# Kernel tuning notes

Hardware: AMD Instinct MI355X
Metric: run time of the kernel (lower is better)

## Reference

```python
import jax, jax.numpy as jnp
import numpy as np

HEADS = 16
DIM_HEAD = 64
SOFTCAP = 50.0
ROPE_THETA = 10000.0


def setup_inputs() -> dict:
    key = jax.random.key(0)
    ks = jax.random.split(key, 5)
    b, n, d, m, lmax = 2, 2048, 1024, 4, 256
    x = jax.random.normal(ks[0], (b, n, d), dtype=jnp.float32)
    tokens = jax.random.normal(ks[1], (b, m, lmax, d), dtype=jnp.float32)
    offsets = jnp.array([100, 600, 1100, 1600], dtype=jnp.int64)
    modalities = jnp.stack(
        [jnp.zeros_like(offsets), offsets, jnp.full_like(offsets, lmax)], axis=-1
    )  # [m, 3] = (type, offset, length)
    modalities = jnp.broadcast_to(modalities, (b, m, 3))
    gamma = jax.random.normal(ks[2], (d,), dtype=jnp.float32) * 0.02
    w_qkv = jax.random.normal(ks[3], (d, 3 * HEADS * DIM_HEAD), dtype=jnp.float32) / np.sqrt(d)
    w_out = jax.random.normal(ks[4], (HEADS * DIM_HEAD, d), dtype=jnp.float32) / np.sqrt(d)
    return {"x": x, "tokens": tokens, "gamma": gamma, "w_qkv": w_qkv,
            "w_out": w_out, "modalities": modalities}


def _apply_rotary(t, pos):
    # t: [b h n dh], pos: [b n] integer rotary positions (interleaved-pair rotation)
    freqs = 1.0 / (ROPE_THETA ** (jnp.arange(0, DIM_HEAD, 2, dtype=jnp.float32) / DIM_HEAD))
    ang = pos[:, None, :, None].astype(jnp.float32) * freqs  # [b 1 n dh/2]
    cos, sin = jnp.cos(ang), jnp.sin(ang)
    t1, t2 = t[..., ::2], t[..., 1::2]
    out = jnp.stack([t1 * cos - t2 * sin, t1 * sin + t2 * cos], axis=-1)
    return out.reshape(t.shape)


def reference(x, tokens, gamma, w_qkv, w_out, modalities):
    b, n, d = x.shape
    lmax = tokens.shape[2]
    off = modalities[..., 1]   # [b m]
    ln = modalities[..., 2]    # [b m]
    seq = jnp.arange(n)

    # --- embed_modality_tokens: scatter modality tokens into sequence ---
    in_span = (seq[None, None, :] >= off[..., None]) & (seq[None, None, :] < (off + ln)[..., None])  # [b m n]
    is_any = in_span.any(axis=1)  # [b n]
    rel = jnp.clip(seq[None, None, :] - off[..., None], 0, lmax - 1)  # [b m n]
    gathered = jnp.take_along_axis(tokens, rel[..., None], axis=2)  # [b m n d]
    mod_embed = jnp.einsum('bmn,bmnd->bnd', in_span.astype(x.dtype), gathered)
    x = jnp.where(is_any[..., None], mod_embed, x)

    # --- derive_rotary_positions_from_modality_positions (offset=[+1,-1]) ---
    rot_span = (seq[None, None, :] >= (off + 1)[..., None]) & (seq[None, None, :] < (off + ln)[..., None])
    pos = seq[None, :] - jnp.cumsum(rot_span.any(axis=1).astype(jnp.int32), axis=-1)  # [b n]

    # --- naive_attn_mask: causal OR within-modality bidirectional ---
    causal = seq[:, None] >= seq[None, :]  # [i j]
    mod_mask = ((seq[None, None, :, None] >= off[..., None, None]) &
                (seq[None, None, None, :] < (off + ln)[..., None, None])).any(axis=1)  # [b i j]
    mask = causal[None] | mod_mask  # [b i j]

    # --- Attention ---
    scale = DIM_HEAD ** -0.5
    xn = x / jnp.clip(jnp.linalg.norm(x, axis=-1, keepdims=True), 1e-12)
    xn = xn * (d ** 0.5) * (gamma + 1.0)  # RMSNorm (l2norm * sqrt(dim) * (gamma+1))
    qkv = (xn @ w_qkv).reshape(b, n, 3, HEADS, DIM_HEAD)
    q, k, v = (jnp.transpose(qkv[:, :, i], (0, 2, 1, 3)) for i in range(3))  # [b h n dh]
    q = _apply_rotary(q, pos)
    k = _apply_rotary(k, pos)
    scores = jnp.einsum('bhid,bhjd->bhij', q, k) * scale
    scores = jnp.tanh(scores / SOFTCAP) * SOFTCAP  # softclamp
    scores = jnp.where(mask[:, None], scores, -jnp.inf)
    attn = jax.nn.softmax(scores, axis=-1)
    out = jnp.einsum('bhij,bhjd->bhid', attn, v)
    out = jnp.transpose(out, (0, 2, 1, 3)).reshape(b, n, HEADS * DIM_HEAD)
    return out @ w_out
```

## Files before the change

kernel.cpp:

```cpp
#include <hip/hip_runtime.h>
#include <stdint.h>

#define HH 16
#define DHD 64
#define BB 2
#define NN 2048
#define DD 1024
#define MMOD 4
#define LMAX 256
#define BNROWS (BB*NN)
#define QKVN (3*HH*DHD)

typedef __attribute__((ext_vector_type(4))) float f32x4;
typedef __attribute__((ext_vector_type(8))) short s16x8;

__device__ __forceinline__ float bf2f(unsigned short b) {
  return __uint_as_float(((unsigned int)b) << 16);
}
__device__ __forceinline__ unsigned short f2bf(float f) {
  unsigned int u = __float_as_uint(f);
  u += 0x7fffu + ((u >> 16) & 1u);
  return (unsigned short)(u >> 16);
}

#define ASYNC_LDS16(g, l) \
  __builtin_amdgcn_global_load_lds((const __attribute__((address_space(1))) void*)(g), \
                                   (__attribute__((address_space(3))) void*)(l), 16, 0, 0)

__global__ __launch_bounds__(256) void k_prep(const float* __restrict__ x,
                                              const float* __restrict__ tokens,
                                              const float* __restrict__ gamma,
                                              const int* __restrict__ mods,
                                              unsigned short* __restrict__ xn) {
  int bs = blockIdx.x;
  int bb = bs / NN, s = bs % NN;
  int t = threadIdx.x;
  int c = t * 4;
  const float4 xv = *(const float4*)(x + (size_t)bs * DD + c);
  float4 acc = {0.f, 0.f, 0.f, 0.f};
  bool any = false;
  #pragma unroll
  for (int m = 0; m < MMOD; ++m) {
    int off = mods[(bb * MMOD + m) * 3 + 1];
    int ln  = mods[(bb * MMOD + m) * 3 + 2];
    if (s >= off && s < off + ln) {
      any = true;
      int rel = s - off;
      if (rel > LMAX - 1) rel = LMAX - 1;
      if (rel < 0) rel = 0;
      const float4 tv = *(const float4*)(tokens + ((size_t)(bb * MMOD + m) * LMAX + rel) * DD + c);
      acc.x += tv.x; acc.y += tv.y; acc.z += tv.z; acc.w += tv.w;
    }
  }
  float4 v = any ? acc : xv;
  float ss = v.x*v.x + v.y*v.y + v.z*v.z + v.w*v.w;
  #pragma unroll
  for (int o = 32; o; o >>= 1) ss += __shfl_xor(ss, o);
  __shared__ float red[4];
  int wv = t >> 6;
  if ((t & 63) == 0) red[wv] = ss;
  __syncthreads();
  float tot = red[0] + red[1] + red[2] + red[3];
  float norm = sqrtf(tot);
  norm = fmaxf(norm, 1e-12f);
  float sc = 32.0f / norm;
  const float4 g = *(const float4*)(gamma + c);
  unsigned long long pk =
      (unsigned long long)f2bf(v.x * sc * (g.x + 1.f)) |
      ((unsigned long long)f2bf(v.y * sc * (g.y + 1.f)) << 16) |
      ((unsigned long long)f2bf(v.z * sc * (g.z + 1.f)) << 32) |
      ((unsigned long long)f2bf(v.w * sc * (g.w + 1.f)) << 48);
  *(unsigned long long*)(xn + (size_t)bs * DD + c) = pk;
}

__global__ void k_pos(const int* __restrict__ mods, int* __restrict__ pos) {
  int bb = blockIdx.x;
  int lane = threadIdx.x;
  int offs[MMOD], ends[MMOD];
  #pragma unroll
  for (int m = 0; m < MMOD; ++m) {
    int off = mods[(bb * MMOD + m) * 3 + 1];
    int ln  = mods[(bb * MMOD + m) * 3 + 2];
    offs[m] = off + 1;
    ends[m] = off + ln;
  }
  int base = lane * (NN / 64);
  int lc[NN / 64];
  int tot = 0;
  #pragma unroll
  for (int i = 0; i < NN / 64; ++i) {
    int s = base + i;
    int f = 0;
    #pragma unroll
    for (int m = 0; m < MMOD; ++m)
      if (s >= offs[m] && s < ends[m]) f = 1;
    tot += f;
    lc[i] = tot;
  }
  int v = tot;
  #pragma unroll
  for (int o = 1; o < 64; o <<= 1) {
    int u = __shfl_up(v, o);
    if (lane >= o) v += u;
  }
  int excl = v - tot;
  #pragma unroll
  for (int i = 0; i < NN / 64; ++i)
    pos[bb * NN + base + i] = base + i - (excl + lc[i]);
}

__global__ void k_tab(const int* __restrict__ pos, float2* __restrict__ tab) {
  int gid = blockIdx.x * 256 + threadIdx.x;
  int p = gid & 31;
  int bs = gid >> 5;
  float inv = expf(-((float)p / 32.f) * 9.210340371976184f);
  float ang = (float)pos[bs] * inv;
  float sn, cs;
  sincosf(ang, &sn, &cs);
  tab[gid] = make_float2(cs, sn);
}

__global__ void k_tr(const float* __restrict__ in, unsigned short* __restrict__ out,
                     int R, int C) {
  __shared__ float tile[32][33];
  int bx = blockIdx.x, by = blockIdx.y;
  int tx = threadIdx.x, ty = threadIdx.y;
  #pragma unroll
  for (int k = 0; k < 4; ++k) {
    int r = by * 32 + ty + k * 8, c = bx * 32 + tx;
    tile[ty + k * 8][tx] = in[(size_t)r * C + c];
  }
  __syncthreads();
  #pragma unroll
  for (int k = 0; k < 4; ++k) {
    int oc = bx * 32 + ty + k * 8;
    int orr = by * 32 + tx;
    out[(size_t)oc * R + orr] = f2bf(tile[tx][ty + k * 8]);
  }
}

template<bool F32OUT>
__global__ __launch_bounds__(256) void k_gemm(const unsigned short* __restrict__ A,
                                              const unsigned short* __restrict__ Bt,
                                              void* __restrict__ Cp,
                                              int M, int Nn, int K) {
  __shared__ unsigned short As[2][128 * 64];
  __shared__ unsigned short Bs[2][128 * 64];
  int tid = threadIdx.x;
  int lane = tid & 63, wv = tid >> 6;
  int lo = lane & 15, hi = lane >> 4;
  int nb = gridDim.x * gridDim.y;
  int fid = blockIdx.y * gridDim.x + blockIdx.x;
  int cpx = nb >> 3;
  int nid = (fid & 7) * cpx + (fid >> 3);
  int m0 = (nid / gridDim.x) * 128;
  int n0 = (nid % gridDim.x) * 128;
  int wr = wv >> 1, wc = wv & 1;
  f32x4 acc[4][4] = {};

  int srow = tid >> 3;
  int scs  = ((tid & 7) ^ ((tid >> 3) & 7)) * 8;
  #define STAGE_G(BUF, KT) do { \
    _Pragma("unroll") \
    for (int is_ = 0; is_ < 4; ++is_) { \
      int r_ = is_ * 32 + srow; \
      const unsigned short* ga_ = A  + (size_t)(m0 + r_) * K + (KT) + scs; \
      const unsigned short* gb_ = Bt + (size_t)(n0 + r_) * K + (KT) + scs; \
      ASYNC_LDS16(ga_, &As[BUF][(is_ * 256 + wv * 64) * 8]); \
      ASYNC_LDS16(gb_, &Bs[BUF][(is_ * 256 + wv * 64) * 8]); \
    } \
  } while (0)

  int nt = K >> 6;
  STAGE_G(0, 0);
  __syncthreads();
  int buf = 0;
  for (int t = 0; t < nt; ++t) {
    if (t + 1 < nt) STAGE_G(buf ^ 1, (t + 1) << 6);
    #pragma unroll
    for (int ks = 0; ks < 2; ++ks) {
      s16x8 af[4], bfr[4];
      #pragma unroll
      for (int m = 0; m < 4; ++m) {
        int row = wr * 64 + m * 16 + lo;
        int cc = ((ks * 4 + hi) ^ (lo & 7)) * 8;
        af[m] = *(const s16x8*)&As[buf][row * 64 + cc];
      }
      #pragma unroll
      for (int nn = 0; nn < 4; ++nn) {
        int row = wc * 64 + nn * 16 + lo;
        int cc = ((ks * 4 + hi) ^ (lo & 7)) * 8;
        bfr[nn] = *(const s16x8*)&Bs[buf][row * 64 + cc];
      }
      #pragma unroll
      for (int m = 0; m < 4; ++m)
        #pragma unroll
        for (int nn = 0; nn < 4; ++nn)
          acc[m][nn] = __builtin_amdgcn_mfma_f32_16x16x32_bf16(af[m], bfr[nn], acc[m][nn], 0, 0, 0);
    }
    __syncthreads();
    buf ^= 1;
  }

  #pragma unroll
  for (int m = 0; m < 4; ++m) {
    #pragma unroll
    for (int nn = 0; nn < 4; ++nn) {
      int r0 = m0 + wr * 64 + m * 16 + hi * 4;
      int cc = n0 + wc * 64 + nn * 16 + lo;
      #pragma unroll
      for (int j = 0; j < 4; ++j) {
        float val = acc[m][nn][j];
        if (F32OUT) ((float*)Cp)[(size_t)(r0 + j) * Nn + cc] = val;
        else        ((unsigned short*)Cp)[(size_t)(r0 + j) * Nn + cc] = f2bf(val);
      }
    }
  }
}

__global__ __launch_bounds__(256) void k_rope(const unsigned short* __restrict__ qkv,
                                              const float2* __restrict__ tab,
                                              unsigned short* __restrict__ q,
                                              unsigned short* __restrict__ k) {
  int bs = blockIdx.x;
  int bb = bs / NN, s = bs % NN;
  int lane = threadIdx.x & 63, wv = threadIdx.x >> 6;
  #pragma unroll
  for (int g = wv; g < 32; g += 4) {
    int i3 = g >> 4, h = g & 15;
    float val = bf2f(qkv[(size_t)bs * QKVN + g * 64 + lane]);
    float partner = __shfl_xor(val, 1);
    float2 cs = tab[(size_t)bs * 32 + (lane >> 1)];
    float out;
    if ((lane & 1) == 0) out = val * cs.x - partner * cs.y;
    else                 out = partner * cs.y + val * cs.x;
    if (i3 == 0) out *= 0.125f;
    unsigned short* dst = (i3 == 0) ? q : k;
    dst[((size_t)(bb * HH + h) * NN + s) * 64 + lane] = f2bf(out);
  }
}

__global__ __launch_bounds__(256) void k_vtr(const unsigned short* __restrict__ qkvt,
                                             unsigned short* __restrict__ vT) {
  __shared__ unsigned short t[64][72];
  int s0 = blockIdx.x * 64, bh = blockIdx.y, bb = bh >> 4, h = bh & 15;
  int tid = threadIdx.x;
  int r = tid >> 2, c0 = (tid & 3) * 16;
  int cw = c0 ^ (((r >> 4) & 3) << 4);
  const unsigned short* src = qkvt + (size_t)(bb * NN + s0 + r) * QKVN + 2048 + h * 64 + c0;
  *(s16x8*)&t[r][cw]     = *(const s16x8*)src;
  *(s16x8*)&t[r][cw + 8] = *(const s16x8*)(src + 8);
  __syncthreads();
  int dh = tid >> 2, sc = (tid & 3) * 16;
  int col2 = dh ^ ((tid & 3) << 4);
  s16x8 o1, o2;
  #pragma unroll
  for (int i = 0; i < 8; ++i) {
    o1[i] = (short)t[sc + i][col2];
    o2[i] = (short)t[sc + 8 + i][col2];
  }
  unsigned short* dst = vT + ((size_t)bh * 64 + dh) * NN + s0 + sc;
  *(s16x8*)dst       = o1;
  *(s16x8*)(dst + 8) = o2;
}

__global__ __launch_bounds__(512) void k_attn(const unsigned short* __restrict__ q,
                                              const unsigned short* __restrict__ k,
                                              const unsigned short* __restrict__ vT,
                                              const int* __restrict__ mods,
                                              unsigned short* __restrict__ o) {
  __shared__ unsigned short Ks[2][64 * 64];
  __shared__ unsigned short Vs[2][64 * 64];
  __shared__ unsigned short Pw[8][16][72];
  int tid = threadIdx.x;
  int lane = tid & 63, wv = tid >> 6;
  int lo = lane & 15, hi = lane >> 4;

  int fid = blockIdx.y * gridDim.x + blockIdx.x;
  int nid = (fid & 7) * 64 + (fid >> 3);
  int bh = nid >> 4;
  int bx = nid & 15;
  int bb = bh >> 4;
  int q0A = (31 - bx) * 64;
  int q0B = bx * 64;
  int q0w = ((wv < 4) ? q0A : q0B) + (wv & 3) * 16;

  const unsigned short* qb = q + (size_t)bh * NN * 64;
  const unsigned short* kb = k + (size_t)bh * NN * 64;
  const unsigned short* vb = vT + (size_t)bh * 64 * NN;

  s16x8 qf[2];
  {
    int qrow = q0w + lo;
    #pragma unroll
    for (int ks = 0; ks < 2; ++ks)
      qf[ks] = *(const s16x8*)&qb[(size_t)qrow * 64 + ks * 32 + hi * 8];
  }

  int off_[MMOD], end_[MMOD];
  #pragma unroll
  for (int m = 0; m < MMOD; ++m) {
    off_[m] = mods[(bb * MMOD + m) * 3 + 1];
    end_[m] = off_[m] + mods[(bb * MMOD + m) * 3 + 2];
  }
  int limit[4];
  #pragma unroll
  for (int j = 0; j < 4; ++j) {
    int r = q0w + hi * 4 + j;
    int L = r + 1;
    #pragma unroll
    for (int m = 0; m < MMOD; ++m)
      if (off_[m] <= r && end_[m] > L) L = end_[m];
    limit[j] = L;
  }
  int minlim, kvmax_w;
  {
    int L = q0w + 1;
    #pragma unroll
    for (int m = 0; m < MMOD; ++m)
      if (off_[m] <= q0w && end_[m] > L) L = end_[m];
    minlim = L;
    int r = q0w + 15;
    int L2 = r + 1;
    #pragma unroll
    for (int m = 0; m < MMOD; ++m)
      if (off_[m] <= r && end_[m] > L2) L2 = end_[m];
    kvmax_w = L2;
  }
  int nt;
  {
    int ra = q0A + 63;
    int LA = ra + 1;
    #pragma unroll
    for (int m = 0; m < MMOD; ++m)
      if (off_[m] <= ra && end_[m] > LA) LA = end_[m];
    int rb2 = q0B + 63;
    int LB = rb2 + 1;
    #pragma unroll
    for (int m = 0; m < MMOD; ++m)
      if (off_[m] <= rb2 && end_[m] > LB) LB = end_[m];
    int Lblk = (LA > LB) ? LA : LB;
    nt = (Lblk + 63) >> 6;
  }

  #define STAGE_KV(B, KV0) do { \
    int r_ = tid >> 3; \
    int cs_ = (lane & 7) ^ ((lane >> 3) & 7); \
    const unsigned short* gK_ = kb + (size_t)((KV0) + r_) * 64 + cs_ * 8; \
    ASYNC_LDS16(gK_, &Ks[B][wv * 512]); \
    const unsigned short* gV_ = vb + (size_t)r_ * NN + (KV0) + cs_ * 8; \
    ASYNC_LDS16(gV_, &Vs[B][wv * 512]); \
  } while (0)

  float lrunp[4] = {0.f, 0.f, 0.f, 0.f};
  f32x4 accO[4] = {};

  STAGE_KV(0, 0);
  __syncthreads();
  int buf = 0;
  for (int t = 0; t < nt; ++t) {
    if (t + 1 < nt) STAGE_KV(buf ^ 1, (t + 1) << 6);
    int kv0 = t << 6;
    if (kv0 < kvmax_w) {
      f32x4 sv[4];
      #pragma unroll
      for (int cb = 0; cb < 4; ++cb) {
        int krow = cb * 16 + lo;
        int c0 = (hi) ^ (krow & 7);
        int c1 = (4 + hi) ^ (krow & 7);
        s16x8 kf0 = *(const s16x8*)&Ks[buf][krow * 64 + c0 * 8];
        s16x8 kf1 = *(const s16x8*)&Ks[buf][krow * 64 + c1 * 8];
        f32x4 z = {};
        z = __builtin_amdgcn_mfma_f32_16x16x32_bf16(qf[0], kf0, z, 0, 0, 0);
        z = __builtin_amdgcn_mfma_f32_16x16x32_bf16(qf[1], kf1, z, 0, 0, 0);
        sv[cb] = z;
      }

      if (kv0 + 64 <= minlim) {
        #pragma unroll
        for (int cb = 0; cb < 4; ++cb)
          #pragma unroll
          for (int j = 0; j < 4; ++j) {
            float s = sv[cb][j];
            float t2 = s * s;
            float u = __builtin_fmaf(t2, -1.3333333e-4f, 1.0f);
            float cap = __builtin_amdgcn_fmed3f(s * u, -50.f, 50.f);
            float p = __expf(cap);
            lrunp[j] += p;
            Pw[wv][hi * 4 + j][cb * 16 + lo] =
                (unsigned short)(__float_as_uint(p) >> 16);
          }
      } else {
        #pragma unroll
        for (int cb = 0; cb < 4; ++cb) {
          int col = kv0 + cb * 16 + lo;
          #pragma unroll
          for (int j = 0; j < 4; ++j) {
            float s = sv[cb][j];
            float t2 = s * s;
            float u = __builtin_fmaf(t2, -1.3333333e-4f, 1.0f);
            float cap = __builtin_amdgcn_fmed3f(s * u, -50.f, 50.f);
            float p = __expf(cap);
            if (col >= limit[j]) p = 0.f;
            lrunp[j] += p;
            Pw[wv][hi * 4 + j][cb * 16 + lo] =
                (unsigned short)(__float_as_uint(p) >> 16);
          }
        }
      }

      #pragma unroll
      for (int ks = 0; ks < 2; ++ks) {
        s16x8 pa = *(const s16x8*)&Pw[wv][lo][ks * 32 + hi * 8];
        #pragma unroll
        for (int cb = 0; cb < 4; ++cb) {
          int vrow = cb * 16 + lo;
          int vc = (ks * 4 + hi) ^ (vrow & 7);
          s16x8 vf = *(const s16x8*)&Vs[buf][vrow * 64 + vc * 8];
          accO[cb] = __builtin_amdgcn_mfma_f32_16x16x32_bf16(pa, vf, accO[cb], 0, 0, 0);
        }
      }
    }
    __syncthreads();
    buf ^= 1;
  }

  #pragma unroll
  for (int o2 = 1; o2 < 16; o2 <<= 1)
    #pragma unroll
    for (int j = 0; j < 4; ++j) lrunp[j] += __shfl_xor(lrunp[j], o2);

  int h = bh & 15;
  float rl[4];
  #pragma unroll
  for (int j = 0; j < 4; ++j) rl[j] = __builtin_amdgcn_rcpf(lrunp[j]);
  #pragma unroll
  for (int cb = 0; cb < 4; ++cb)
    #pragma unroll
    for (int j = 0; j < 4; ++j) {
      int r = q0w + hi * 4 + j;
      float val = accO[cb][j] * rl[j];
      o[((size_t)(bb * NN) + r) * (HH * DHD) + h * 64 + cb * 16 + lo] = f2bf(val);
    }
}

extern "C" void kernel_launch(void* const* d_in, const int* in_sizes, int n_in,
                              void* d_out, int out_size, void* d_ws, size_t ws_size,
                              hipStream_t stream) {
  (void)in_sizes; (void)n_in; (void)out_size; (void)ws_size;
  const float* x      = (const float*)d_in[0];
  const float* tokens = (const float*)d_in[1];
  const float* gamma  = (const float*)d_in[2];
  const float* w_qkv  = (const float*)d_in[3];
  const float* w_out  = (const float*)d_in[4];
  const int*   mods   = (const int*)d_in[5];

  char* ws = (char*)d_ws;
  unsigned short* xn    = (unsigned short*)(ws + 0);
  unsigned short* wqkvT = (unsigned short*)(ws + 8388608);
  unsigned short* woutT = (unsigned short*)(ws + 14680064);
  unsigned short* qkvt  = (unsigned short*)(ws + 16777216);
  unsigned short* qd    = (unsigned short*)(ws + 41943040);
  unsigned short* kd    = (unsigned short*)(ws + 50331648);
  unsigned short* vTd   = (unsigned short*)(ws + 58720256);
  unsigned short* attno = (unsigned short*)(ws + 67108864);
  int*            pos   = (int*)(ws + 75497472);
  float2*         tab   = (float2*)(ws + 75513856);

  k_prep<<<BNROWS, 256, 0, stream>>>(x, tokens, gamma, mods, xn);
  k_pos<<<BB, 64, 0, stream>>>(mods, pos);
  k_tab<<<(BB * NN * 32) / 256, 256, 0, stream>>>(pos, tab);
  k_tr<<<dim3(QKVN / 32, DD / 32), dim3(32, 8), 0, stream>>>(w_qkv, wqkvT, DD, QKVN);
  k_tr<<<dim3((HH * DHD) / 32, DD / 32), dim3(32, 8), 0, stream>>>(w_out, woutT, HH * DHD, DD);
  k_gemm<false><<<dim3(QKVN / 128, BNROWS / 128), 256, 0, stream>>>(xn, wqkvT, (void*)qkvt, BNROWS, QKVN, DD);
  k_rope<<<BNROWS, 256, 0, stream>>>(qkvt, tab, qd, kd);
  k_vtr<<<dim3(NN / 64, BB * HH), 256, 0, stream>>>(qkvt, vTd);
  k_attn<<<dim3(16, BB * HH), 512, 0, stream>>>(qd, kd, vTd, mods, attno);
  k_gemm<true><<<dim3(DD / 128, BNROWS / 128), 256, 0, stream>>>(attno, woutT, d_out, BNROWS, DD, DD);
}
```

Before: 138.3 us.

## Keep attention probabilities in registers via transposed QK MFMA, dropping LDS P staging

```diff
diff --git a/kernel.cpp b/kernel.cpp
--- a/kernel.cpp
+++ b/kernel.cpp
@@ -13,6 +13,7 @@
 
 typedef __attribute__((ext_vector_type(4))) float f32x4;
 typedef __attribute__((ext_vector_type(8))) short s16x8;
+typedef __attribute__((ext_vector_type(4))) short s16x4;
 
 __device__ __forceinline__ float bf2f(unsigned short b) {
   return __uint_as_float(((unsigned int)b) << 16);
@@ -21,6 +22,11 @@
   unsigned int u = __float_as_uint(f);
   u += 0x7fffu + ((u >> 16) & 1u);
   return (unsigned short)(u >> 16);
+}
+__device__ __forceinline__ unsigned int cvt_pk_bf16(float a, float b) {
+  unsigned int r;
+  asm("v_cvt_pk_bf16_f32 %0, %1, %2" : "=v"(r) : "v"(a), "v"(b));
+  return r;
 }
 
 #define ASYNC_LDS16(g, l) \
@@ -234,7 +240,7 @@
     float out;
     if ((lane & 1) == 0) out = val * cs.x - partner * cs.y;
     else                 out = partner * cs.y + val * cs.x;
-    if (i3 == 0) out *= 0.125f;
+    if (i3 == 0) out *= 0.18033688011112042f;
     unsigned short* dst = (i3 == 0) ? q : k;
     dst[((size_t)(bb * HH + h) * NN + s) * 64 + lane] = f2bf(out);
   }
@@ -271,7 +277,6 @@
                                               unsigned short* __restrict__ o) {
   __shared__ unsigned short Ks[2][64 * 64];
   __shared__ unsigned short Vs[2][64 * 64];
-  __shared__ unsigned short Pw[8][16][72];
   int tid = threadIdx.x;
   int lane = tid & 63, wv = tid >> 6;
   int lo = lane & 15, hi = lane >> 4;
@@ -303,15 +308,14 @@
     off_[m] = mods[(bb * MMOD + m) * 3 + 1];
     end_[m] = off_[m] + mods[(bb * MMOD + m) * 3 + 2];
   }
-  int limit[4];
-  #pragma unroll
-  for (int j = 0; j < 4; ++j) {
-    int r = q0w + hi * 4 + j;
+  int limit_l;
+  {
+    int r = q0w + lo;
     int L = r + 1;
     #pragma unroll
     for (int m = 0; m < MMOD; ++m)
       if (off_[m] <= r && end_[m] > L) L = end_[m];
-    limit[j] = L;
+    limit_l = L;
   }
   int minlim, kvmax_w;
   {
@@ -352,7 +356,7 @@
     ASYNC_LDS16(gV_, &Vs[B][wv * 512]); \
   } while (0)
 
-  float lrunp[4] = {0.f, 0.f, 0.f, 0.f};
+  float lr = 0.f;
   f32x4 accO[4] = {};
 
   STAGE_KV(0, 0);
@@ -363,6 +367,7 @@
     int kv0 = t << 6;
     if (kv0 < kvmax_w) {
       f32x4 sv[4];
+      __builtin_amdgcn_s_setprio(1);
       #pragma unroll
       for (int cb = 0; cb < 4; ++cb) {
         int krow = cb * 16 + lo;
@@ -371,69 +376,67 @@
         s16x8 kf0 = *(const s16x8*)&Ks[buf][krow * 64 + c0 * 8];
         s16x8 kf1 = *(const s16x8*)&Ks[buf][krow * 64 + c1 * 8];
         f32x4 z = {};
-        z = __builtin_amdgcn_mfma_f32_16x16x32_bf16(qf[0], kf0, z, 0, 0, 0);
-        z = __builtin_amdgcn_mfma_f32_16x16x32_bf16(qf[1], kf1, z, 0, 0, 0);
+        z = __builtin_amdgcn_mfma_f32_16x16x32_bf16(kf0, qf[0], z, 0, 0, 0);
+        z = __builtin_amdgcn_mfma_f32_16x16x32_bf16(kf1, qf[1], z, 0, 0, 0);
         sv[cb] = z;
       }
-
-      if (kv0 + 64 <= minlim) {
+      __builtin_amdgcn_s_setprio(0);
+
+      unsigned int pk_[4][2];
+      bool edge = (kv0 + 64 > minlim);
+      int kb0 = kv0 + hi * 4;
+      #pragma unroll
+      for (int cb = 0; cb < 4; ++cb) {
+        float p[4];
         #pragma unroll
-        for (int cb = 0; cb < 4; ++cb)
-          #pragma unroll
-          for (int j = 0; j < 4; ++j) {
-            float s = sv[cb][j];
-            float t2 = s * s;
-            float u = __builtin_fmaf(t2, -1.3333333e-4f, 1.0f);
-            float cap = __builtin_amdgcn_fmed3f(s * u, -50.f, 50.f);
-            float p = __expf(cap);
-            lrunp[j] += p;
-            Pw[wv][hi * 4 + j][cb * 16 + lo] =
-                (unsigned short)(__float_as_uint(p) >> 16);
-          }
-      } else {
+        for (int j = 0; j < 4; ++j) {
+          float s = sv[cb][j];
+          float u = __builtin_fmaf(s * s, -6.40604e-5f, 1.0f);
+          float pp = __builtin_amdgcn_exp2f(s * u);
+          if (edge && (kb0 + cb * 16 + j) >= limit_l) pp = 0.f;
+          p[j] = pp;
+        }
+        lr += (p[0] + p[1]) + (p[2] + p[3]);
+        pk_[cb][0] = cvt_pk_bf16(p[0], p[1]);
+        pk_[cb][1] = cvt_pk_bf16(p[2], p[3]);
+      }
+
+      union { unsigned int u[4]; s16x8 v; } pa0, pa1;
+      pa0.u[0] = pk_[0][0]; pa0.u[1] = pk_[0][1];
+      pa0.u[2] = pk_[1][0]; pa0.u[3] = pk_[1][1];
+      pa1.u[0] = pk_[2][0]; pa1.u[1] = pk_[2][1];
+      pa1.u[2] = pk_[3][0]; pa1.u[3] = pk_[3][1];
+
+      __builtin_amdgcn_s_setprio(1);
+      #pragma unroll
+      for (int ks = 0; ks < 2; ++ks) {
+        s16x8 pa = ks ? pa1.v : pa0.v;
+        int c16 = 4 * ks + (hi >> 1);
+        int sub = (hi & 1) * 4;
         #pragma unroll
-        for (int cb = 0; cb < 4; ++cb) {
-          int col = kv0 + cb * 16 + lo;
-          #pragma unroll
-          for (int j = 0; j < 4; ++j) {
-            float s = sv[cb][j];
-            float t2 = s * s;
-            float u = __builtin_fmaf(t2, -1.3333333e-4f, 1.0f);
-            float cap = __builtin_amdgcn_fmed3f(s * u, -50.f, 50.f);
-            float p = __expf(cap);
-            if (col >= limit[j]) p = 0.f;
-            lrunp[j] += p;
-            Pw[wv][hi * 4 + j][cb * 16 + lo] =
-                (unsigned short)(__float_as_uint(p) >> 16);
-          }
+        for (int cbo = 0; cbo < 4; ++cbo) {
+          int dh = cbo * 16 + lo;
+          int base = dh * 64 + sub;
+          s16x4 vA = *(const s16x4*)&Vs[buf][base + ((c16 ^ (dh & 7)) << 3)];
+          s16x4 vB = *(const s16x4*)&Vs[buf][base + (((c16 + 2) ^ (dh & 7)) << 3)];
+          s16x8 vf = __builtin_shufflevector(vA, vB, 0, 1, 2, 3, 4, 5, 6, 7);
+          accO[cbo] = __builtin_amdgcn_mfma_f32_16x16x32_bf16(pa, vf, accO[cbo], 0, 0, 0);
         }
       }
-
-      #pragma unroll
-      for (int ks = 0; ks < 2; ++ks) {
-        s16x8 pa = *(const s16x8*)&Pw[wv][lo][ks * 32 + hi * 8];
-        #pragma unroll
-        for (int cb = 0; cb < 4; ++cb) {
-          int vrow = cb * 16 + lo;
-          int vc = (ks * 4 + hi) ^ (vrow & 7);
-          s16x8 vf = *(const s16x8*)&Vs[buf][vrow * 64 + vc * 8];
-          accO[cb] = __builtin_amdgcn_mfma_f32_16x16x32_bf16(pa, vf, accO[cb], 0, 0, 0);
-        }
-      }
+      __builtin_amdgcn_s_setprio(0);
     }
     __syncthreads();
     buf ^= 1;
   }
 
-  #pragma unroll
-  for (int o2 = 1; o2 < 16; o2 <<= 1)
-    #pragma unroll
-    for (int j = 0; j < 4; ++j) lrunp[j] += __shfl_xor(lrunp[j], o2);
+  lr += __shfl_xor(lr, 16);
+  lr += __shfl_xor(lr, 32);
+  float rl[4];
+  #pragma unroll
+  for (int j = 0; j < 4; ++j)
+    rl[j] = __builtin_amdgcn_rcpf(__shfl(lr, hi * 4 + j));
 
   int h = bh & 15;
-  float rl[4];
-  #pragma unroll
-  for (int j = 0; j < 4; ++j) rl[j] = __builtin_amdgcn_rcpf(lrunp[j]);
   #pragma unroll
   for (int cb = 0; cb < 4; ++cb)
     #pragma unroll
```

Result: slower. 141.7 us (+2.4%).
